# Kernel tuning notes

Hardware: AMD Instinct MI355X
Metric: run time of the kernel (lower is better)

## Reference

```python
import jax, jax.numpy as jnp
import numpy as np

MARGIN = 0.3
BIG = 10000.0  # sentinel used by the original when a gt/lt negative set is empty


def setup_inputs() -> dict:
    key = jax.random.key(0)
    k1, k2 = jax.random.split(key)
    inputs = jax.random.normal(k1, (4096, 256), dtype=jnp.float32)
    targets = jax.random.randint(k2, (4096,), 0, 4, dtype=jnp.int32)
    return {"inputs": inputs, "targets": targets}


def reference(inputs, targets):
    # Pairwise Euclidean distance matrix (n, n).
    sq = jnp.sum(inputs * inputs, axis=1)
    d2 = sq[:, None] + sq[None, :] - 2.0 * (inputs @ inputs.T)
    dist = jnp.sqrt(jnp.maximum(d2, 0.0))

    # mask[i, j] semantics from the torch code (rows of expand are `targets`):
    #   eq: targets[j] == targets[i]; gt: targets[j] > targets[i]; lt: targets[j] < targets[i]
    eq = targets[None, :] == targets[:, None]
    gt = targets[None, :] > targets[:, None]
    lt = targets[None, :] < targets[:, None]

    # Hardest positive: max distance over same-label columns (diag always eq -> non-empty).
    hard_ap = jnp.max(jnp.where(eq, dist, -jnp.inf), axis=1)
    # Hardest greater / less negatives: min distance, sentinel BIG when set empty.
    an_g = jnp.min(jnp.where(gt, dist, jnp.inf), axis=1)
    an_g = jnp.where(jnp.isinf(an_g), BIG, an_g)
    an_l = jnp.min(jnp.where(lt, dist, jnp.inf), axis=1)
    an_l = jnp.where(jnp.isinf(an_l), BIG, an_l)

    loss = jnp.mean(jax.nn.relu(hard_ap - jnp.abs(an_g - an_l) + MARGIN))
    # cnt: rows whose positive set is just the anchor itself
    cnt = jnp.sum(jnp.sum(eq, axis=1) == 1)
    return loss, dist, cnt
```

## Files before the change

### kernel.cpp

```cpp
#include <hip/hip_runtime.h>

#define N 4096
#define D 256
#define MARGIN 0.3f
#define BIG 10000.0f

typedef _Float16 f16x8 __attribute__((ext_vector_type(8)));
typedef _Float16 f16x4 __attribute__((ext_vector_type(4)));
typedef float floatx16 __attribute__((ext_vector_type(16)));

__device__ inline void atomicMaxFloatPos(float* a, float v) {
    atomicMax((int*)a, __float_as_int(v));
}
__device__ inline void atomicMinFloatPos(float* a, float v) {
    atomicMin((int*)a, __float_as_int(v));
}

__device__ inline void gl_lds16(const void* g, void* l) {
    __builtin_amdgcn_global_load_lds(
        (const __attribute__((address_space(1))) unsigned int*)g,
        (__attribute__((address_space(3))) unsigned int*)l, 16, 0, 0);
}

__global__ __launch_bounds__(256) void prep_kernel(const float* __restrict__ x,
                                                   float* __restrict__ sq,
                                                   _Float16* __restrict__ Xf,
                                                   float* ap, float* ang, float* anl) {
    const int wave = threadIdx.x >> 6, lane = threadIdx.x & 63;
    const int row = blockIdx.x * 4 + wave;
    const float4 v = *(const float4*)(x + (size_t)row * D + lane * 4);
    f16x4 h;
    h[0] = (_Float16)v.x; h[1] = (_Float16)v.y;
    h[2] = (_Float16)v.z; h[3] = (_Float16)v.w;
    *(f16x4*)(Xf + (size_t)row * D + lane * 4) = h;
    const float c0 = (float)h[0], c1 = (float)h[1], c2 = (float)h[2], c3 = (float)h[3];
    float s = c0 * c0 + c1 * c1 + c2 * c2 + c3 * c3;
    #pragma unroll
    for (int off = 32; off; off >>= 1) s += __shfl_down(s, off);
    if (lane == 0) sq[row] = s;
    if (threadIdx.x < 4) {
        const int i = blockIdx.x * 4 + threadIdx.x;
        ap[i] = 0.0f; ang[i] = BIG; anl[i] = BIG;
    }
}

__global__ __launch_bounds__(256, 4) void dist_kernel(const _Float16* __restrict__ Xf,
                                                      const int* __restrict__ tgt,
                                                      const float* __restrict__ sq,
                                                      float* __restrict__ dist,
                                                      float* ap, float* ang, float* anl) {
    __shared__ _Float16 lds[16384];

    const int tid  = threadIdx.x;
    const int wv   = tid >> 6;
    const int lane = tid & 63;
    const int row0 = blockIdx.y * 128;
    const int col0 = blockIdx.x * 128;
    const int wr = wv >> 1, wc = wv & 1;

    const int g = lane >> 3, p = lane & 7, lq = p ^ g;
    const int selrow = (wv < 2 ? row0 : col0) + (wv & 1) * 64 + g;
    const _Float16* src0 = Xf + (size_t)selrow * D + lq * 8;
    _Float16* dst0 = lds + wv * 8 * 512;

    const int m0 = lane & 31;
    const int hi = lane >> 5;
    const int sw = m0 & 7;
    const int rowbase = row0 + wr * 64;
    const int colbase = col0 + wc * 64;
    const int tl = tgt[rowbase + lane];
    const float sq_r = sq[rowbase + lane];
    const unsigned long long pb0 = __ballot(tl & 1);
    const unsigned long long pb1 = __ballot(tl & 2);
    const int gc0 = colbase + m0, gc1 = colbase + 32 + m0;
    const int tc0 = tgt[gc0], tc1 = tgt[gc1];
    const float sqc0 = sq[gc0], sqc1 = sq[gc1];

    floatx16 acc[2][2];
    #pragma unroll
    for (int mt = 0; mt < 2; ++mt)
        #pragma unroll
        for (int nt = 0; nt < 2; ++nt)
            #pragma unroll
            for (int r = 0; r < 16; ++r) acc[mt][nt][r] = 0.0f;

    const _Float16* ldsA0 = lds + (wr * 64 + m0) * 64;
    const _Float16* ldsA1 = lds + (wr * 64 + 32 + m0) * 64;
    const _Float16* ldsB0 = lds + 8192 + (wc * 64 + m0) * 64;
    const _Float16* ldsB1 = lds + 8192 + (wc * 64 + 32 + m0) * 64;

    #pragma unroll
    for (int s = 0; s < 4; ++s) {
        if (s) {
            __asm__ volatile("s_waitcnt lgkmcnt(0)" ::: "memory");
            __builtin_amdgcn_s_barrier();
        }
        const int k0 = s * 64;
        #pragma unroll
        for (int d = 0; d < 8; ++d)
            gl_lds16(src0 + (size_t)d * 8 * D + k0, dst0 + d * 512);
        __asm__ volatile("s_waitcnt vmcnt(0)" ::: "memory");
        __builtin_amdgcn_s_barrier();

        __builtin_amdgcn_s_setprio(1);
        #pragma unroll
        for (int ks = 0; ks < 4; ++ks) {
            const int la = ks * 2 + hi;
            const int po = (la ^ sw) << 3;
            f16x8 a0 = *(const f16x8*)(ldsA0 + po);
            f16x8 a1 = *(const f16x8*)(ldsA1 + po);
            f16x8 b0 = *(const f16x8*)(ldsB0 + po);
            f16x8 b1 = *(const f16x8*)(ldsB1 + po);
            acc[0][0] = __builtin_amdgcn_mfma_f32_32x32x16_f16(a0, b0, acc[0][0], 0, 0, 0);
            acc[0][1] = __builtin_amdgcn_mfma_f32_32x32x16_f16(a0, b1, acc[0][1], 0, 0, 0);
            acc[1][0] = __builtin_amdgcn_mfma_f32_32x32x16_f16(a1, b0, acc[1][0], 0, 0, 0);
            acc[1][1] = __builtin_amdgcn_mfma_f32_32x32x16_f16(a1, b1, acc[1][1], 0, 0, 0);
        }
        __builtin_amdgcn_s_setprio(0);
        __asm__ volatile("" ::: "memory");
    }

    const int rl_base = 4 * hi;

    float mx0 = 0.0f, mg0 = BIG, ml0 = BIG;
    float mx1 = 0.0f, mg1 = BIG, ml1 = BIG;

    #pragma unroll
    for (int mt = 0; mt < 2; ++mt) {
        #pragma unroll
        for (int r = 0; r < 16; ++r) {
            const int row_l = mt * 32 + (r & 3) + 8 * (r >> 2) + rl_base;
            const int grow  = rowbase + row_l;
            const float sqi = __shfl(sq_r, row_l);
            const float d0 = sqrtf(fmaxf(sqi + sqc0 - 2.0f * acc[mt][0][r], 0.0f));
            const float d1 = sqrtf(fmaxf(sqi + sqc1 - 2.0f * acc[mt][1][r], 0.0f));
            __builtin_nontemporal_store(d0, dist + (size_t)grow * N + gc0);
            __builtin_nontemporal_store(d1, dist + (size_t)grow * N + gc1);
            const int tr = (int)((pb0 >> row_l) & 1) | ((int)((pb1 >> row_l) & 1) << 1);
            mx0 = fmaxf(mx0, (tr == tc0) ? d0 : 0.0f);
            mg0 = fminf(mg0, (tr >  tc0) ? d0 : BIG);
            ml0 = fminf(ml0, (tr <  tc0) ? d0 : BIG);
            mx1 = fmaxf(mx1, (tr == tc1) ? d1 : 0.0f);
            mg1 = fminf(mg1, (tr >  tc1) ? d1 : BIG);
            ml1 = fminf(ml1, (tr <  tc1) ? d1 : BIG);
        }
    }
    mx0 = fmaxf(mx0, __shfl_xor(mx0, 32));
    mg0 = fminf(mg0, __shfl_xor(mg0, 32));
    ml0 = fminf(ml0, __shfl_xor(ml0, 32));
    mx1 = fmaxf(mx1, __shfl_xor(mx1, 32));
    mg1 = fminf(mg1, __shfl_xor(mg1, 32));
    ml1 = fminf(ml1, __shfl_xor(ml1, 32));

    if (hi == 0) {
        atomicMaxFloatPos(&ap[gc0],  mx0);
        atomicMinFloatPos(&ang[gc0], mg0);
        atomicMinFloatPos(&anl[gc0], ml0);
        atomicMaxFloatPos(&ap[gc1],  mx1);
        atomicMinFloatPos(&ang[gc1], mg1);
        atomicMinFloatPos(&anl[gc1], ml1);
    }
}

__global__ __launch_bounds__(1024) void finish_kernel(const float* __restrict__ ap,
                                                      const float* __restrict__ ang,
                                                      const float* __restrict__ anl,
                                                      const int* __restrict__ tgt,
                                                      float* __restrict__ out) {
    __shared__ int hist[4];
    __shared__ unsigned hsum[2][16];
    __shared__ float wsum[16];
    __shared__ int wcnt[16];
    const int tid = threadIdx.x, lane = tid & 63, wv = tid >> 6;

    const int4 t4 = *(const int4*)&tgt[tid * 4];
    int c[4] = {0, 0, 0, 0};
    c[t4.x & 3]++; c[t4.y & 3]++; c[t4.z & 3]++; c[t4.w & 3]++;
    unsigned p01 = (unsigned)c[0] | ((unsigned)c[1] << 16);
    unsigned p23 = (unsigned)c[2] | ((unsigned)c[3] << 16);
    #pragma unroll
    for (int off = 32; off; off >>= 1) {
        p01 += __shfl_down(p01, off);
        p23 += __shfl_down(p23, off);
    }
    if (lane == 0) { hsum[0][wv] = p01; hsum[1][wv] = p23; }
    __syncthreads();
    if (tid == 0) {
        unsigned a = 0, b = 0;
        for (int i = 0; i < 16; ++i) { a += hsum[0][i]; b += hsum[1][i]; }
        hist[0] = a & 0xFFFF; hist[1] = a >> 16;
        hist[2] = b & 0xFFFF; hist[3] = b >> 16;
    }
    __syncthreads();

    float term = 0.0f; int cc = 0;
    const int lab[4] = {t4.x & 3, t4.y & 3, t4.z & 3, t4.w & 3};
    #pragma unroll
    for (int j = 0; j < 4; ++j) {
        const int i = tid * 4 + j;
        term += fmaxf(ap[i] - fabsf(ang[i] - anl[i]) + MARGIN, 0.0f);
        cc += (hist[lab[j]] == 1) ? 1 : 0;
    }
    #pragma unroll
    for (int off = 32; off; off >>= 1) {
        term += __shfl_down(term, off);
        cc   += __shfl_down(cc, off);
    }
    if (lane == 0) { wsum[wv] = term; wcnt[wv] = cc; }
    __syncthreads();
    if (tid == 0) {
        float ls = 0.0f; int cs = 0;
        for (int i = 0; i < 16; ++i) { ls += wsum[i]; cs += wcnt[i]; }
        out[0] = ls * (1.0f / N);
        out[1 + (size_t)N * N] = (float)cs;
    }
}

extern "C" void kernel_launch(void* const* d_in, const int* in_sizes, int n_in,
                              void* d_out, int out_size, void* d_ws, size_t ws_size,
                              hipStream_t stream) {
    const float* x   = (const float*)d_in[0];
    const int*   tgt = (const int*)d_in[1];
    float* out = (float*)d_out;
    char*  ws  = (char*)d_ws;

    _Float16* Xf  = (_Float16*)ws;
    float*    sq  = (float*)(ws + 2097152);
    float*    ap  = sq + 4096;
    float*    ang = sq + 8192;
    float*    anl = sq + 12288;

    prep_kernel<<<N / 4, 256, 0, stream>>>(x, sq, Xf, ap, ang, anl);
    dim3 grid(N / 128, N / 128);
    dist_kernel<<<grid, 256, 0, stream>>>(Xf, tgt, sq, out + 1, ap, ang, anl);
    finish_kernel<<<1, 1024, 0, stream>>>(ap, ang, anl, tgt, out);
}
```

Before: 113.2 us.

## Pre-swizzle fp16 operands into MFMA fragment layout and load directly from global

The prep kernel now writes the fp16 copy of the inputs in a blocked layout that matches the MFMA 32x32x16 operand fragments: 32-row blocks by 16 k-blocks of 512 halves. The distance kernel drops the LDS staging, the global_load_lds copies and the barriers, and each wave loads its A and B fragments straight from global memory with contiguous 16-byte loads. This removes LDS traffic and synchronisation, but operands shared between waves are now fetched redundantly from L2 rather than reused through LDS.

```diff
diff --git a/kernel.cpp b/kernel.cpp
--- a/kernel.cpp
+++ b/kernel.cpp
@@ -14,12 +14,6 @@
 }
 __device__ inline void atomicMinFloatPos(float* a, float v) {
     atomicMin((int*)a, __float_as_int(v));
-}
-
-__device__ inline void gl_lds16(const void* g, void* l) {
-    __builtin_amdgcn_global_load_lds(
-        (const __attribute__((address_space(1))) unsigned int*)g,
-        (__attribute__((address_space(3))) unsigned int*)l, 16, 0, 0);
 }
 
 __global__ __launch_bounds__(256) void prep_kernel(const float* __restrict__ x,
@@ -32,7 +26,9 @@
     f16x4 h;
     h[0] = (_Float16)v.x; h[1] = (_Float16)v.y;
     h[2] = (_Float16)v.z; h[3] = (_Float16)v.w;
-    *(f16x4*)(Xf + (size_t)row * D + lane * 4) = h;
+    const int kb = lane >> 2, hi = (lane >> 1) & 1, j0 = (lane & 1) * 4;
+    const size_t dst = ((size_t)(row >> 5) * 16 + kb) * 512 + (hi * 32 + (row & 31)) * 8 + j0;
+    *(f16x4*)(Xf + dst) = h;
     const float c0 = (float)h[0], c1 = (float)h[1], c2 = (float)h[2], c3 = (float)h[3];
     float s = c0 * c0 + c1 * c1 + c2 * c2 + c3 * c3;
     #pragma unroll
@@ -49,8 +45,6 @@
                                                       const float* __restrict__ sq,
                                                       float* __restrict__ dist,
                                                       float* ap, float* ang, float* anl) {
-    __shared__ _Float16 lds[16384];
-
     const int tid  = threadIdx.x;
     const int wv   = tid >> 6;
     const int lane = tid & 63;
@@ -58,20 +52,21 @@
     const int col0 = blockIdx.x * 128;
     const int wr = wv >> 1, wc = wv & 1;
 
-    const int g = lane >> 3, p = lane & 7, lq = p ^ g;
-    const int selrow = (wv < 2 ? row0 : col0) + (wv & 1) * 64 + g;
-    const _Float16* src0 = Xf + (size_t)selrow * D + lq * 8;
-    _Float16* dst0 = lds + wv * 8 * 512;
+    const int RB0 = blockIdx.y * 4 + wr * 2;
+    const int CB0 = blockIdx.x * 4 + wc * 2;
+    const _Float16* pa0 = Xf + (size_t)RB0 * 16 * 512 + lane * 8;
+    const _Float16* pa1 = pa0 + 16 * 512;
+    const _Float16* pb0 = Xf + (size_t)CB0 * 16 * 512 + lane * 8;
+    const _Float16* pb1 = pb0 + 16 * 512;
 
     const int m0 = lane & 31;
     const int hi = lane >> 5;
-    const int sw = m0 & 7;
     const int rowbase = row0 + wr * 64;
     const int colbase = col0 + wc * 64;
     const int tl = tgt[rowbase + lane];
     const float sq_r = sq[rowbase + lane];
-    const unsigned long long pb0 = __ballot(tl & 1);
-    const unsigned long long pb1 = __ballot(tl & 2);
+    const unsigned long long pb_0 = __ballot(tl & 1);
+    const unsigned long long pb_1 = __ballot(tl & 2);
     const int gc0 = colbase + m0, gc1 = colbase + 32 + m0;
     const int tc0 = tgt[gc0], tc1 = tgt[gc1];
     const float sqc0 = sq[gc0], sqc1 = sq[gc1];
@@ -84,40 +79,16 @@
             #pragma unroll
             for (int r = 0; r < 16; ++r) acc[mt][nt][r] = 0.0f;
 
-    const _Float16* ldsA0 = lds + (wr * 64 + m0) * 64;
-    const _Float16* ldsA1 = lds + (wr * 64 + 32 + m0) * 64;
-    const _Float16* ldsB0 = lds + 8192 + (wc * 64 + m0) * 64;
-    const _Float16* ldsB1 = lds + 8192 + (wc * 64 + 32 + m0) * 64;
-
-    #pragma unroll
-    for (int s = 0; s < 4; ++s) {
-        if (s) {
-            __asm__ volatile("s_waitcnt lgkmcnt(0)" ::: "memory");
-            __builtin_amdgcn_s_barrier();
-        }
-        const int k0 = s * 64;
-        #pragma unroll
-        for (int d = 0; d < 8; ++d)
-            gl_lds16(src0 + (size_t)d * 8 * D + k0, dst0 + d * 512);
-        __asm__ volatile("s_waitcnt vmcnt(0)" ::: "memory");
-        __builtin_amdgcn_s_barrier();
-
-        __builtin_amdgcn_s_setprio(1);
-        #pragma unroll
-        for (int ks = 0; ks < 4; ++ks) {
-            const int la = ks * 2 + hi;
-            const int po = (la ^ sw) << 3;
-            f16x8 a0 = *(const f16x8*)(ldsA0 + po);
-            f16x8 a1 = *(const f16x8*)(ldsA1 + po);
-            f16x8 b0 = *(const f16x8*)(ldsB0 + po);
-            f16x8 b1 = *(const f16x8*)(ldsB1 + po);
-            acc[0][0] = __builtin_amdgcn_mfma_f32_32x32x16_f16(a0, b0, acc[0][0], 0, 0, 0);
-            acc[0][1] = __builtin_amdgcn_mfma_f32_32x32x16_f16(a0, b1, acc[0][1], 0, 0, 0);
-            acc[1][0] = __builtin_amdgcn_mfma_f32_32x32x16_f16(a1, b0, acc[1][0], 0, 0, 0);
-            acc[1][1] = __builtin_amdgcn_mfma_f32_32x32x16_f16(a1, b1, acc[1][1], 0, 0, 0);
-        }
-        __builtin_amdgcn_s_setprio(0);
-        __asm__ volatile("" ::: "memory");
+    #pragma unroll
+    for (int kb = 0; kb < 16; ++kb) {
+        const f16x8 a0 = *(const f16x8*)(pa0 + kb * 512);
+        const f16x8 a1 = *(const f16x8*)(pa1 + kb * 512);
+        const f16x8 b0 = *(const f16x8*)(pb0 + kb * 512);
+        const f16x8 b1 = *(const f16x8*)(pb1 + kb * 512);
+        acc[0][0] = __builtin_amdgcn_mfma_f32_32x32x16_f16(a0, b0, acc[0][0], 0, 0, 0);
+        acc[0][1] = __builtin_amdgcn_mfma_f32_32x32x16_f16(a0, b1, acc[0][1], 0, 0, 0);
+        acc[1][0] = __builtin_amdgcn_mfma_f32_32x32x16_f16(a1, b0, acc[1][0], 0, 0, 0);
+        acc[1][1] = __builtin_amdgcn_mfma_f32_32x32x16_f16(a1, b1, acc[1][1], 0, 0, 0);
     }
 
     const int rl_base = 4 * hi;
@@ -136,7 +107,7 @@
             const float d1 = sqrtf(fmaxf(sqi + sqc1 - 2.0f * acc[mt][1][r], 0.0f));
             __builtin_nontemporal_store(d0, dist + (size_t)grow * N + gc0);
             __builtin_nontemporal_store(d1, dist + (size_t)grow * N + gc1);
-            const int tr = (int)((pb0 >> row_l) & 1) | ((int)((pb1 >> row_l) & 1) << 1);
+            const int tr = (int)((pb_0 >> row_l) & 1) | ((int)((pb_1 >> row_l) & 1) << 1);
             mx0 = fmaxf(mx0, (tr == tc0) ? d0 : 0.0f);
             mg0 = fminf(mg0, (tr >  tc0) ? d0 : BIG);
             ml0 = fminf(ml0, (tr <  tc0) ? d0 : BIG);
```

New measurement: 115.3 us. No clear change (+1.8%).

## Enlarge distance tile to 256x256 with 8 waves and double-buffered LDS

Applied to the files above, without the earlier changes.

The distance GEMM block tile grows from 128x128 to 256x256, using 512 threads. Each wave now computes a 128x64 sub-tile from 8 MFMA accumulators, so each B fragment loaded from LDS is reused across four A fragments. LDS is double-buffered, so the load for the next K stage is issued before the current stage is computed, overlapping global-to-LDS copies with MFMA work. The cost is 128KB of LDS per block, which allows only one block per CU, and a grid of just 256 blocks. That lower occupancy may expose latency in the store-heavy epilogue that writes the distance matrix.

```diff
diff --git a/kernel.cpp b/kernel.cpp
--- a/kernel.cpp
+++ b/kernel.cpp
@@ -44,99 +44,114 @@
     }
 }
 
-__global__ __launch_bounds__(256, 4) void dist_kernel(const _Float16* __restrict__ Xf,
+__global__ __launch_bounds__(512, 2) void dist_kernel(const _Float16* __restrict__ Xf,
                                                       const int* __restrict__ tgt,
                                                       const float* __restrict__ sq,
                                                       float* __restrict__ dist,
                                                       float* ap, float* ang, float* anl) {
-    __shared__ _Float16 lds[16384];
+    __shared__ _Float16 lds[65536];
 
     const int tid  = threadIdx.x;
     const int wv   = tid >> 6;
     const int lane = tid & 63;
-    const int row0 = blockIdx.y * 128;
-    const int col0 = blockIdx.x * 128;
-    const int wr = wv >> 1, wc = wv & 1;
+    const int row0 = blockIdx.y * 256;
+    const int col0 = blockIdx.x * 256;
+    const int wr = wv >> 2, wc = wv & 3;
 
     const int g = lane >> 3, p = lane & 7, lq = p ^ g;
-    const int selrow = (wv < 2 ? row0 : col0) + (wv & 1) * 64 + g;
-    const _Float16* src0 = Xf + (size_t)selrow * D + lq * 8;
-    _Float16* dst0 = lds + wv * 8 * 512;
+    const int base_row = (wv < 4 ? row0 : col0) + (wv & 3) * 64 + g;
+    const _Float16* src0 = Xf + (size_t)base_row * D + lq * 8;
+    const int dstoff = ((wv & 4) ? 16384 : 0) + (wv & 3) * 4096;
 
     const int m0 = lane & 31;
     const int hi = lane >> 5;
     const int sw = m0 & 7;
-    const int rowbase = row0 + wr * 64;
-    const int colbase = col0 + wc * 64;
-    const int tl = tgt[rowbase + lane];
-    const float sq_r = sq[rowbase + lane];
-    const unsigned long long pb0 = __ballot(tl & 1);
-    const unsigned long long pb1 = __ballot(tl & 2);
-    const int gc0 = colbase + m0, gc1 = colbase + 32 + m0;
-    const int tc0 = tgt[gc0], tc1 = tgt[gc1];
-    const float sqc0 = sq[gc0], sqc1 = sq[gc1];
-
-    floatx16 acc[2][2];
-    #pragma unroll
-    for (int mt = 0; mt < 2; ++mt)
+
+    floatx16 acc[4][2];
+    #pragma unroll
+    for (int mt = 0; mt < 4; ++mt)
         #pragma unroll
         for (int nt = 0; nt < 2; ++nt)
             #pragma unroll
             for (int r = 0; r < 16; ++r) acc[mt][nt][r] = 0.0f;
 
-    const _Float16* ldsA0 = lds + (wr * 64 + m0) * 64;
-    const _Float16* ldsA1 = lds + (wr * 64 + 32 + m0) * 64;
-    const _Float16* ldsB0 = lds + 8192 + (wc * 64 + m0) * 64;
-    const _Float16* ldsB1 = lds + 8192 + (wc * 64 + 32 + m0) * 64;
+    #define ISSUE_STAGE(s)                                                        \
+    do {                                                                          \
+        _Float16* buf_ = lds + ((s) & 1) * 32768;                                 \
+        const int k0_ = (s) * 64;                                                 \
+        _Pragma("unroll")                                                         \
+        for (int d = 0; d < 8; ++d)                                               \
+            gl_lds16(src0 + (size_t)d * 8 * D + k0_, buf_ + dstoff + d * 512);    \
+    } while (0)
+
+    ISSUE_STAGE(0);
 
     #pragma unroll
     for (int s = 0; s < 4; ++s) {
-        if (s) {
-            __asm__ volatile("s_waitcnt lgkmcnt(0)" ::: "memory");
-            __builtin_amdgcn_s_barrier();
-        }
-        const int k0 = s * 64;
-        #pragma unroll
-        for (int d = 0; d < 8; ++d)
-            gl_lds16(src0 + (size_t)d * 8 * D + k0, dst0 + d * 512);
-        __asm__ volatile("s_waitcnt vmcnt(0)" ::: "memory");
+        if (s < 3) ISSUE_STAGE(s + 1);
+        if (s < 3) { __asm__ volatile("s_waitcnt vmcnt(8)" ::: "memory"); }
+        else       { __asm__ volatile("s_waitcnt vmcnt(0)" ::: "memory"); }
         __builtin_amdgcn_s_barrier();
+        __asm__ volatile("" ::: "memory");
+
+        const _Float16* buf   = lds + (s & 1) * 32768;
+        const _Float16* Abase = buf + ((size_t)wr * 8192 + m0 * 64);
+        const _Float16* Bbase = buf + 16384 + ((size_t)wc * 4096 + m0 * 64);
 
         __builtin_amdgcn_s_setprio(1);
         #pragma unroll
-        for (int ks = 0; ks < 4; ++ks) {
-            const int la = ks * 2 + hi;
-            const int po = (la ^ sw) << 3;
-            f16x8 a0 = *(const f16x8*)(ldsA0 + po);
-            f16x8 a1 = *(const f16x8*)(ldsA1 + po);
-            f16x8 b0 = *(const f16x8*)(ldsB0 + po);
-            f16x8 b1 = *(const f16x8*)(ldsB1 + po);
-            acc[0][0] = __builtin_amdgcn_mfma_f32_32x32x16_f16(a0, b0, acc[0][0], 0, 0, 0);
-            acc[0][1] = __builtin_amdgcn_mfma_f32_32x32x16_f16(a0, b1, acc[0][1], 0, 0, 0);
-            acc[1][0] = __builtin_amdgcn_mfma_f32_32x32x16_f16(a1, b0, acc[1][0], 0, 0, 0);
-            acc[1][1] = __builtin_amdgcn_mfma_f32_32x32x16_f16(a1, b1, acc[1][1], 0, 0, 0);
+        for (int kb = 0; kb < 4; ++kb) {
+            const int po = (((kb * 2 + hi) ^ sw) << 3);
+            f16x8 b0 = *(const f16x8*)(Bbase + po);
+            f16x8 b1 = *(const f16x8*)(Bbase + 2048 + po);
+            #pragma unroll
+            for (int mt = 0; mt < 4; ++mt) {
+                f16x8 a = *(const f16x8*)(Abase + mt * 2048 + po);
+                acc[mt][0] = __builtin_amdgcn_mfma_f32_32x32x16_f16(a, b0, acc[mt][0], 0, 0, 0);
+                acc[mt][1] = __builtin_amdgcn_mfma_f32_32x32x16_f16(a, b1, acc[mt][1], 0, 0, 0);
+            }
         }
         __builtin_amdgcn_s_setprio(0);
-        __asm__ volatile("" ::: "memory");
-    }
-
+
+        if (s < 2) {
+            __asm__ volatile("" ::: "memory");
+            __builtin_amdgcn_s_barrier();
+            __asm__ volatile("" ::: "memory");
+        }
+    }
+    #undef ISSUE_STAGE
+
+    const int rowA    = row0 + wr * 128;
+    const int colbase = col0 + wc * 64;
+    const int tl0 = tgt[rowA + lane];
+    const int tl1 = tgt[rowA + 64 + lane];
+    const float sqr0 = sq[rowA + lane];
+    const float sqr1 = sq[rowA + 64 + lane];
+    const unsigned long long pa0 = __ballot(tl0 & 1), pa1 = __ballot(tl0 & 2);
+    const unsigned long long pb0 = __ballot(tl1 & 1), pb1 = __ballot(tl1 & 2);
+    const int gc0 = colbase + m0, gc1 = colbase + 32 + m0;
+    const int tc0 = tgt[gc0], tc1 = tgt[gc1];
+    const float sqc0 = sq[gc0], sqc1 = sq[gc1];
     const int rl_base = 4 * hi;
 
     float mx0 = 0.0f, mg0 = BIG, ml0 = BIG;
     float mx1 = 0.0f, mg1 = BIG, ml1 = BIG;
 
     #pragma unroll
-    for (int mt = 0; mt < 2; ++mt) {
+    for (int mt = 0; mt < 4; ++mt) {
         #pragma unroll
         for (int r = 0; r < 16; ++r) {
             const int row_l = mt * 32 + (r & 3) + 8 * (r >> 2) + rl_base;
-            const int grow  = rowbase + row_l;
-            const float sqi = __shfl(sq_r, row_l);
+            const int rl = row_l & 63;
+            const int grow = rowA + row_l;
+            const float sqi = __shfl(mt < 2 ? sqr0 : sqr1, rl);
             const float d0 = sqrtf(fmaxf(sqi + sqc0 - 2.0f * acc[mt][0][r], 0.0f));
             const float d1 = sqrtf(fmaxf(sqi + sqc1 - 2.0f * acc[mt][1][r], 0.0f));
             __builtin_nontemporal_store(d0, dist + (size_t)grow * N + gc0);
             __builtin_nontemporal_store(d1, dist + (size_t)grow * N + gc1);
-            const int tr = (int)((pb0 >> row_l) & 1) | ((int)((pb1 >> row_l) & 1) << 1);
+            const unsigned long long q0 = (mt < 2 ? pa0 : pb0);
+            const unsigned long long q1 = (mt < 2 ? pa1 : pb1);
+            const int tr = (int)((q0 >> rl) & 1) | ((int)((q1 >> rl) & 1) << 1);
             mx0 = fmaxf(mx0, (tr == tc0) ? d0 : 0.0f);
             mg0 = fminf(mg0, (tr >  tc0) ? d0 : BIG);
             ml0 = fminf(ml0, (tr <  tc0) ? d0 : BIG);
@@ -231,7 +246,7 @@
     float*    anl = sq + 12288;
 
     prep_kernel<<<N / 4, 256, 0, stream>>>(x, sq, Xf, ap, ang, anl);
-    dim3 grid(N / 128, N / 128);
-    dist_kernel<<<grid, 256, 0, stream>>>(Xf, tgt, sq, out + 1, ap, ang, anl);
+    dim3 grid(N / 256, N / 256);
+    dist_kernel<<<grid, 512, 0, stream>>>(Xf, tgt, sq, out + 1, ap, ang, anl);
     finish_kernel<<<1, 1024, 0, stream>>>(ap, ang, anl, tgt, out);
 }
```

Result: faster. 108.9 us (-3.8%).

## Exploit distance matrix symmetry by computing only upper-triangular tiles

Applied to the files above, without the earlier changes.

The launch now covers only the 528 upper-triangular 128x128 tiles instead of all 1024, decoding the tile coordinates with a square-root formula. For each off-diagonal tile, the wave transposes its results through LDS, writes the mirrored block, and updates the row-wise reductions for the other side via atomics. This roughly halves the MFMA work and the operand loads. The cost is extra LDS traffic, a barrier, more atomics and a strided transposed store pattern, and the kernel was likely dominated by writing the 64 MB output anyway.

```diff
diff --git a/kernel.cpp b/kernel.cpp
--- a/kernel.cpp
+++ b/kernel.cpp
@@ -54,8 +54,16 @@
     const int tid  = threadIdx.x;
     const int wv   = tid >> 6;
     const int lane = tid & 63;
-    const int row0 = blockIdx.y * 128;
-    const int col0 = blockIdx.x * 128;
+
+    const int idx = blockIdx.x;
+    int bx = (int)((sqrtf(8.0f * (float)idx + 1.0f) - 1.0f) * 0.5f);
+    while ((bx + 1) * (bx + 2) / 2 <= idx) ++bx;
+    while (bx * (bx + 1) / 2 > idx) --bx;
+    const int by = idx - bx * (bx + 1) / 2;
+    const int row0 = by * 128;
+    const int col0 = bx * 128;
+    const bool diag = (by == bx);
+
     const int wr = wv >> 1, wc = wv & 1;
 
     const int g = lane >> 3, p = lane & 7, lq = p ^ g;
@@ -68,10 +76,13 @@
     const int sw = m0 & 7;
     const int rowbase = row0 + wr * 64;
     const int colbase = col0 + wc * 64;
-    const int tl = tgt[rowbase + lane];
+    const int tl  = tgt[rowbase + lane];
+    const int tcl = tgt[colbase + lane];
     const float sq_r = sq[rowbase + lane];
-    const unsigned long long pb0 = __ballot(tl & 1);
-    const unsigned long long pb1 = __ballot(tl & 2);
+    const unsigned long long pb_0 = __ballot(tl & 1);
+    const unsigned long long pb_1 = __ballot(tl & 2);
+    const unsigned long long pc_0 = __ballot(tcl & 1);
+    const unsigned long long pc_1 = __ballot(tcl & 2);
     const int gc0 = colbase + m0, gc1 = colbase + 32 + m0;
     const int tc0 = tgt[gc0], tc1 = tgt[gc1];
     const float sqc0 = sq[gc0], sqc1 = sq[gc1];
@@ -121,6 +132,12 @@
     }
 
     const int rl_base = 4 * hi;
+    float* Tph = (float*)lds + wv * 2048;
+
+    if (!diag) {
+        __asm__ volatile("s_waitcnt lgkmcnt(0)" ::: "memory");
+        __builtin_amdgcn_s_barrier();
+    }
 
     float mx0 = 0.0f, mg0 = BIG, ml0 = BIG;
     float mx1 = 0.0f, mg1 = BIG, ml1 = BIG;
@@ -136,13 +153,45 @@
             const float d1 = sqrtf(fmaxf(sqi + sqc1 - 2.0f * acc[mt][1][r], 0.0f));
             __builtin_nontemporal_store(d0, dist + (size_t)grow * N + gc0);
             __builtin_nontemporal_store(d1, dist + (size_t)grow * N + gc1);
-            const int tr = (int)((pb0 >> row_l) & 1) | ((int)((pb1 >> row_l) & 1) << 1);
+            const int tr = (int)((pb_0 >> row_l) & 1) | ((int)((pb_1 >> row_l) & 1) << 1);
             mx0 = fmaxf(mx0, (tr == tc0) ? d0 : 0.0f);
             mg0 = fminf(mg0, (tr >  tc0) ? d0 : BIG);
             ml0 = fminf(ml0, (tr <  tc0) ? d0 : BIG);
             mx1 = fmaxf(mx1, (tr == tc1) ? d1 : 0.0f);
             mg1 = fminf(mg1, (tr >  tc1) ? d1 : BIG);
             ml1 = fminf(ml1, (tr <  tc1) ? d1 : BIG);
+            if (!diag) {
+                const int rr = row_l & 31;
+                Tph[rr * 64 + ((m0 ^ rr) & 63)]        = d0;
+                Tph[rr * 64 + (((32 + m0) ^ rr) & 63)] = d1;
+            }
+        }
+        if (!diag) {
+            float mxT = 0.0f, mgT = BIG, mlT = BIG;
+            const int tra = __shfl(tl, mt * 32 + m0);
+            #pragma unroll
+            for (int mtc = 0; mtc < 2; ++mtc) {
+                #pragma unroll
+                for (int r = 0; r < 16; ++r) {
+                    const int crow = mtc * 32 + (r & 3) + 8 * (r >> 2) + rl_base;
+                    const float v = Tph[m0 * 64 + ((crow ^ m0) & 63)];
+                    __builtin_nontemporal_store(
+                        v, dist + (size_t)(colbase + crow) * N + rowbase + mt * 32 + m0);
+                    const int tcr = (int)((pc_0 >> crow) & 1) | ((int)((pc_1 >> crow) & 1) << 1);
+                    mxT = fmaxf(mxT, (tcr == tra) ? v : 0.0f);
+                    mgT = fminf(mgT, (tcr >  tra) ? v : BIG);
+                    mlT = fminf(mlT, (tcr <  tra) ? v : BIG);
+                }
+            }
+            mxT = fmaxf(mxT, __shfl_xor(mxT, 32));
+            mgT = fminf(mgT, __shfl_xor(mgT, 32));
+            mlT = fminf(mlT, __shfl_xor(mlT, 32));
+            if (hi == 0) {
+                const int a = rowbase + mt * 32 + m0;
+                atomicMaxFloatPos(&ap[a],  mxT);
+                atomicMinFloatPos(&ang[a], mgT);
+                atomicMinFloatPos(&anl[a], mlT);
+            }
         }
     }
     mx0 = fmaxf(mx0, __shfl_xor(mx0, 32));
@@ -231,7 +280,7 @@
     float*    anl = sq + 12288;
 
     prep_kernel<<<N / 4, 256, 0, stream>>>(x, sq, Xf, ap, ang, anl);
-    dim3 grid(N / 128, N / 128);
-    dist_kernel<<<grid, 256, 0, stream>>>(Xf, tgt, sq, out + 1, ap, ang, anl);
+    const int ntiles = (N / 128) * (N / 128 + 1) / 2;
+    dist_kernel<<<ntiles, 256, 0, stream>>>(Xf, tgt, sq, out + 1, ap, ang, anl);
     finish_kernel<<<1, 1024, 0, stream>>>(ap, ang, anl, tgt, out);
 }
```

Result: slower. 198.2 us (+75.1%).
